# Optimization experiments

Measured on AMD Instinct MI355X. Metric: run time of the kernel, lower is better.

## Reference

```python
import jax, jax.numpy as jnp
import numpy as np

MARGIN = 0.2


def _pairwise_distances(emb):
    # Euclidean distances with torch-style zero-masked sqrt (non-squared path).
    dot = jnp.matmul(emb, emb.T)                      # [N, N]
    sq = jnp.diagonal(dot)                            # [N]
    d2 = sq[None, :] - 2.0 * dot + sq[:, None]
    d2 = jnp.maximum(d2, 0.0)
    zero_mask = (d2 == 0.0).astype(d2.dtype)
    return (1.0 - zero_mask) * jnp.sqrt(d2 + zero_mask * 1e-16)


def setup_inputs() -> dict:
    key = jax.random.key(0)
    k1, k2 = jax.random.split(key)
    N, D, C = 512, 512, 64
    labels = jax.random.randint(k1, (N,), 0, C, dtype=jnp.int64 if jax.config.jax_enable_x64 else jnp.int32)
    embeddings = jax.random.normal(k2, (N, D), dtype=jnp.float32)
    return {"labels": labels, "embeddings": embeddings}


def reference(labels, embeddings):
    # Semi-hard... actually Difficulty.Easy path of TripletLoss.forward
    N = embeddings.shape[0]
    pdist = _pairwise_distances(embeddings)                      # [N, N]
    adjacency_not = labels[None, :] != labels[:, None]           # [N, N] bool

    pdist_tile = jnp.tile(pdist, (N, 1))                         # [N*N, N]
    mask = jnp.tile(adjacency_not, (N, 1))                       # [N*N, N]
    # Easy difficulty: negatives strictly farther than the anchor-positive dist
    mask = mask & (pdist_tile > pdist.T.reshape(-1, 1))

    maskf = mask.astype(pdist.dtype)
    mask_final = (jnp.sum(maskf, axis=1, keepdims=True) > 0.0).reshape(N, N).T  # [N, N] bool

    # masked minimum over tiled rows
    axis_max = jnp.max(pdist_tile, axis=1, keepdims=True)
    neg_outside = (jnp.min((pdist_tile - axis_max) * maskf, axis=1, keepdims=True)
                   + axis_max).reshape(N, N).T                   # [N, N]

    # masked maximum over negatives per anchor
    adjf = adjacency_not.astype(pdist.dtype)
    axis_min = jnp.min(pdist, axis=1, keepdims=True)
    neg_inside = jnp.max((pdist - axis_min) * adjf, axis=1, keepdims=True) + axis_min  # [N, 1]
    neg_inside = jnp.broadcast_to(neg_inside, (N, N))

    semi_hard_negatives = jnp.where(mask_final, neg_outside, neg_inside)
    loss_mat = MARGIN + pdist - semi_hard_negatives

    eye = jnp.eye(N, dtype=bool)
    mask_positives = (labels[None, :] == labels[:, None]) & ~eye
    num_positives = jnp.sum(mask_positives).astype(loss_mat.dtype)
    loss = jnp.sum(jnp.maximum(loss_mat * mask_positives.astype(loss_mat.dtype), 0.0))
    return loss / (num_positives + 1e-8)
```

## Files before the change

kernel.cpp:

```cpp
#include <hip/hip_runtime.h>
#include <math.h>


#define NN 512
#define DD 512
#define JT 2
#define TPB 512
#define NWAVES (TPB / 64)
#define DC 64
#define NCHUNK (DD / DC)
#define LSTR (DC + 4)
#define NF4 (DC / 4)
#define MARGIN_F 0.2f

__global__ __launch_bounds__(TPB) void triplet_main(
    const int* __restrict__ labels,
    const float* __restrict__ emb,
    float* __restrict__ part_loss,
    int* __restrict__ part_cnt)
{
    __shared__ float bch[NN * LSTR];
    __shared__ float dist[JT][NN];
    __shared__ int slbl[NN];
    __shared__ unsigned short plist[JT][NN];
    __shared__ int pcnt[JT];
    __shared__ float snorm[JT];
    __shared__ float bloss;

    const int tid = threadIdx.x;
    const int j0 = blockIdx.x * JT;

    slbl[tid] = labels[tid];
    if (tid < JT) pcnt[tid] = 0;
    if (tid == 0) bloss = 0.f;

    float g0 = 0.f, g1 = 0.f, ss = 0.f;

    for (int c = 0; c < NCHUNK; ++c) {
        __syncthreads();
        #pragma unroll
        for (int u = 0; u < (NN * NF4) / TPB; ++u) {
            const int idx = tid + u * TPB;
            const int r  = idx >> 4;
            const int c4 = idx & 15;
            float4 v = *(const float4*)(emb + (size_t)r * DD + c * DC + (c4 << 2));
            *(float4*)(&bch[r * LSTR + (c4 << 2)]) = v;
        }
        __syncthreads();
        const float4* own = (const float4*)(&bch[tid * LSTR]);
        const float4* a0p = (const float4*)(&bch[j0 * LSTR]);
        const float4* a1p = (const float4*)(&bch[(j0 + 1) * LSTR]);
        #pragma unroll 8
        for (int i = 0; i < NF4; ++i) {
            const float4 x  = own[i];
            const float4 a0 = a0p[i];
            const float4 a1 = a1p[i];
            g0 = fmaf(a0.x, x.x, g0); g0 = fmaf(a0.y, x.y, g0);
            g0 = fmaf(a0.z, x.z, g0); g0 = fmaf(a0.w, x.w, g0);
            g1 = fmaf(a1.x, x.x, g1); g1 = fmaf(a1.y, x.y, g1);
            g1 = fmaf(a1.z, x.z, g1); g1 = fmaf(a1.w, x.w, g1);
            ss = fmaf(x.x, x.x, ss);  ss = fmaf(x.y, x.y, ss);
            ss = fmaf(x.z, x.z, ss);  ss = fmaf(x.w, x.w, ss);
        }
    }

    if (tid == j0)     snorm[0] = ss;
    if (tid == j0 + 1) snorm[1] = ss;
    __syncthreads();
    {
        const float s0 = snorm[0], s1 = snorm[1];
        const float d20 = fmaxf(s0 + ss - 2.f * g0, 0.f);
        const float d21 = fmaxf(s1 + ss - 2.f * g1, 0.f);
        dist[0][tid] = sqrtf(d20);
        dist[1][tid] = sqrtf(d21);
    }
    __syncthreads();

    #pragma unroll
    for (int r = 0; r < JT; ++r) {
        const int j = j0 + r;
        if (tid != j && slbl[tid] == slbl[j]) {
            const int idx = atomicAdd(&pcnt[r], 1);
            plist[r][idx] = (unsigned short)tid;
        }
    }
    __syncthreads();

    const int wave = tid >> 6;
    const int lane = tid & 63;
    float wloss = 0.f;
    for (int r = 0; r < JT; ++r) {
        const int lbl = slbl[j0 + r];
        const int np = pcnt[r];
        for (int p = wave; p < np; p += NWAVES) {
            const int a = plist[r][p];
            const float dpa = dist[r][a];
            float vmin = 1e30f;
            float vmax = 0.f;
            #pragma unroll
            for (int i = 0; i < NN / 64; ++i) {
                const int k = lane + (i << 6);
                const float dk = dist[r][k];
                if (slbl[k] != lbl) {
                    vmax = fmaxf(vmax, dk);
                    if (dk > dpa) vmin = fminf(vmin, dk);
                }
            }
            #pragma unroll
            for (int o = 32; o > 0; o >>= 1) {
                vmin = fminf(vmin, __shfl_xor(vmin, o, 64));
                vmax = fmaxf(vmax, __shfl_xor(vmax, o, 64));
            }
            const float negd = (vmin < 1e29f) ? vmin : vmax;
            const float term = MARGIN_F + dpa - negd;
            if (lane == 0 && term > 0.f) wloss += term;
        }
    }
    if (lane == 0 && wloss != 0.f) atomicAdd(&bloss, wloss);
    __syncthreads();
    if (tid == 0) {
        part_loss[blockIdx.x] = bloss;
        part_cnt[blockIdx.x]  = pcnt[0] + pcnt[1];
    }
}

__global__ __launch_bounds__(256) void triplet_finalize(
    const float* __restrict__ part_loss,
    const int* __restrict__ part_cnt,
    float* __restrict__ out)
{
    __shared__ float sl[4];
    __shared__ int sc[4];
    const int tid = threadIdx.x;
    float L = part_loss[tid];
    int   c = part_cnt[tid];
    #pragma unroll
    for (int o = 32; o > 0; o >>= 1) {
        L += __shfl_xor(L, o, 64);
        c += __shfl_xor(c, o, 64);
    }
    if ((tid & 63) == 0) { sl[tid >> 6] = L; sc[tid >> 6] = c; }
    __syncthreads();
    if (tid == 0) {
        const float Ls = sl[0] + sl[1] + sl[2] + sl[3];
        const float cs = (float)(sc[0] + sc[1] + sc[2] + sc[3]);
        out[0] = Ls / (cs + 1e-8f);
    }
}

extern "C" void kernel_launch(void* const* d_in, const int* in_sizes, int n_in,
                              void* d_out, int out_size, void* d_ws, size_t ws_size,
                              hipStream_t stream) {
    const int* labels = (const int*)d_in[0];
    const float* emb  = (const float*)d_in[1];
    float* part_loss = (float*)d_ws;
    int*   part_cnt  = (int*)((char*)d_ws + (NN / JT) * sizeof(float));

    triplet_main<<<NN / JT, TPB, 0, stream>>>(labels, emb, part_loss, part_cnt);
    triplet_finalize<<<1, 256, 0, stream>>>(part_loss, part_cnt, (float*)d_out);
}
```

Baseline: 83.57 us.

## Compute distances directly from global memory with register-held anchor rows

Removes the large shared-memory staging of the whole embedding matrix and its per-chunk barriers. Each block now keeps its two anchor rows in registers and has groups of 8 lanes compute squared differences directly against rows read from global memory, reducing them with shuffles. This replaces the Gram-matrix-plus-norms formula with a direct difference form. The smaller shared footprint and a launch bound of 2 blocks per CU are meant to raise occupancy, at the cost of more register pressure and every block reading the full matrix from cache.

```diff
diff --git a/kernel.cpp b/kernel.cpp
--- a/kernel.cpp
+++ b/kernel.cpp
@@ -3,104 +3,92 @@
 
 
 #define NN 512
-#define DD 512
-#define JT 2
 #define TPB 512
 #define NWAVES (TPB / 64)
-#define DC 64
-#define NCHUNK (DD / DC)
-#define LSTR (DC + 4)
-#define NF4 (DC / 4)
 #define MARGIN_F 0.2f
 
-__global__ __launch_bounds__(TPB) void triplet_main(
+__global__ __launch_bounds__(TPB, 2) void triplet_main(
     const int* __restrict__ labels,
     const float* __restrict__ emb,
     float* __restrict__ part_loss,
     int* __restrict__ part_cnt)
 {
-    __shared__ float bch[NN * LSTR];
-    __shared__ float dist[JT][NN];
+    __shared__ float dist[2][NN];
     __shared__ int slbl[NN];
-    __shared__ unsigned short plist[JT][NN];
-    __shared__ int pcnt[JT];
-    __shared__ float snorm[JT];
+    __shared__ unsigned short plist[2][NN];
+    __shared__ int pcnt[2];
     __shared__ float bloss;
 
-    const int tid = threadIdx.x;
-    const int j0 = blockIdx.x * JT;
+    const int tid  = threadIdx.x;
+    const int lane = tid & 63;
+    const int wave = tid >> 6;
+    const int s = lane & 7;
+    const int r = lane >> 3;
+    const int j0 = blockIdx.x * 2;
 
     slbl[tid] = labels[tid];
-    if (tid < JT) pcnt[tid] = 0;
+    if (tid < 2) pcnt[tid] = 0;
     if (tid == 0) bloss = 0.f;
 
-    float g0 = 0.f, g1 = 0.f, ss = 0.f;
+    const float4* ef4 = (const float4*)emb;
 
-    for (int c = 0; c < NCHUNK; ++c) {
-        __syncthreads();
-        #pragma unroll
-        for (int u = 0; u < (NN * NF4) / TPB; ++u) {
-            const int idx = tid + u * TPB;
-            const int r  = idx >> 4;
-            const int c4 = idx & 15;
-            float4 v = *(const float4*)(emb + (size_t)r * DD + c * DC + (c4 << 2));
-            *(float4*)(&bch[r * LSTR + (c4 << 2)]) = v;
-        }
-        __syncthreads();
-        const float4* own = (const float4*)(&bch[tid * LSTR]);
-        const float4* a0p = (const float4*)(&bch[j0 * LSTR]);
-        const float4* a1p = (const float4*)(&bch[(j0 + 1) * LSTR]);
-        #pragma unroll 8
-        for (int i = 0; i < NF4; ++i) {
-            const float4 x  = own[i];
-            const float4 a0 = a0p[i];
-            const float4 a1 = a1p[i];
-            g0 = fmaf(a0.x, x.x, g0); g0 = fmaf(a0.y, x.y, g0);
-            g0 = fmaf(a0.z, x.z, g0); g0 = fmaf(a0.w, x.w, g0);
-            g1 = fmaf(a1.x, x.x, g1); g1 = fmaf(a1.y, x.y, g1);
-            g1 = fmaf(a1.z, x.z, g1); g1 = fmaf(a1.w, x.w, g1);
-            ss = fmaf(x.x, x.x, ss);  ss = fmaf(x.y, x.y, ss);
-            ss = fmaf(x.z, x.z, ss);  ss = fmaf(x.w, x.w, ss);
-        }
+    float4 A0[16], A1[16];
+    #pragma unroll
+    for (int i = 0; i < 16; ++i) {
+        A0[i] = ef4[(size_t)j0 * 128 + (i << 3) + s];
+        A1[i] = ef4[(size_t)(j0 + 1) * 128 + (i << 3) + s];
     }
 
-    if (tid == j0)     snorm[0] = ss;
-    if (tid == j0 + 1) snorm[1] = ss;
-    __syncthreads();
-    {
-        const float s0 = snorm[0], s1 = snorm[1];
-        const float d20 = fmaxf(s0 + ss - 2.f * g0, 0.f);
-        const float d21 = fmaxf(s1 + ss - 2.f * g1, 0.f);
-        dist[0][tid] = sqrtf(d20);
-        dist[1][tid] = sqrtf(d21);
+    for (int g = 0; g < 8; ++g) {
+        const int krow = (wave << 6) + (g << 3) + r;
+        const float4* rowp = ef4 + (size_t)krow * 128 + s;
+        float acc0 = 0.f, acc1 = 0.f;
+        #pragma unroll
+        for (int i = 0; i < 16; ++i) {
+            const float4 e = rowp[i << 3];
+            float t;
+            t = A0[i].x - e.x; acc0 = fmaf(t, t, acc0);
+            t = A0[i].y - e.y; acc0 = fmaf(t, t, acc0);
+            t = A0[i].z - e.z; acc0 = fmaf(t, t, acc0);
+            t = A0[i].w - e.w; acc0 = fmaf(t, t, acc0);
+            t = A1[i].x - e.x; acc1 = fmaf(t, t, acc1);
+            t = A1[i].y - e.y; acc1 = fmaf(t, t, acc1);
+            t = A1[i].z - e.z; acc1 = fmaf(t, t, acc1);
+            t = A1[i].w - e.w; acc1 = fmaf(t, t, acc1);
+        }
+        acc0 += __shfl_xor(acc0, 1, 64); acc1 += __shfl_xor(acc1, 1, 64);
+        acc0 += __shfl_xor(acc0, 2, 64); acc1 += __shfl_xor(acc1, 2, 64);
+        acc0 += __shfl_xor(acc0, 4, 64); acc1 += __shfl_xor(acc1, 4, 64);
+        if (s == 0) {
+            dist[0][krow] = sqrtf(acc0);
+            dist[1][krow] = sqrtf(acc1);
+        }
     }
     __syncthreads();
 
     #pragma unroll
-    for (int r = 0; r < JT; ++r) {
-        const int j = j0 + r;
+    for (int rr = 0; rr < 2; ++rr) {
+        const int j = j0 + rr;
         if (tid != j && slbl[tid] == slbl[j]) {
-            const int idx = atomicAdd(&pcnt[r], 1);
-            plist[r][idx] = (unsigned short)tid;
+            const int idx = atomicAdd(&pcnt[rr], 1);
+            plist[rr][idx] = (unsigned short)tid;
         }
     }
     __syncthreads();
 
-    const int wave = tid >> 6;
-    const int lane = tid & 63;
     float wloss = 0.f;
-    for (int r = 0; r < JT; ++r) {
-        const int lbl = slbl[j0 + r];
-        const int np = pcnt[r];
+    for (int rr = 0; rr < 2; ++rr) {
+        const int lbl = slbl[j0 + rr];
+        const int np = pcnt[rr];
         for (int p = wave; p < np; p += NWAVES) {
-            const int a = plist[r][p];
-            const float dpa = dist[r][a];
+            const int a = plist[rr][p];
+            const float dpa = dist[rr][a];
             float vmin = 1e30f;
             float vmax = 0.f;
             #pragma unroll
             for (int i = 0; i < NN / 64; ++i) {
                 const int k = lane + (i << 6);
-                const float dk = dist[r][k];
+                const float dk = dist[rr][k];
                 if (slbl[k] != lbl) {
                     vmax = fmaxf(vmax, dk);
                     if (dk > dpa) vmin = fminf(vmin, dk);
@@ -154,8 +142,8 @@
     const int* labels = (const int*)d_in[0];
     const float* emb  = (const float*)d_in[1];
     float* part_loss = (float*)d_ws;
-    int*   part_cnt  = (int*)((char*)d_ws + (NN / JT) * sizeof(float));
+    int*   part_cnt  = (int*)((char*)d_ws + 256 * sizeof(float));
 
-    triplet_main<<<NN / JT, TPB, 0, stream>>>(labels, emb, part_loss, part_cnt);
+    triplet_main<<<NN / 2, TPB, 0, stream>>>(labels, emb, part_loss, part_cnt);
     triplet_finalize<<<1, 256, 0, stream>>>(part_loss, part_cnt, (float*)d_out);
 }
```

New measurement: 105.1 us. +25.8%, slower.
